# Kernel tuning notes

Hardware: AMD Instinct MI355X
Metric: run time of the kernel (lower is better)

Reference implementation:

```python
import jax, jax.numpy as jnp
import numpy as np

DECAY = 0.99
EPS = 1e-5


def setup_inputs() -> dict:
    key = jax.random.key(0)
    k1, k2 = jax.random.split(key)
    inp = jax.random.normal(k1, (32, 64, 64, 64), dtype=jnp.float32)  # [B,H,W,dim]
    embed = jax.random.normal(k2, (64, 512), dtype=jnp.float32)       # [dim, n_embed]
    cluster_size = jnp.zeros((512,), dtype=jnp.float32)
    embed_avg = embed  # buffer initialized as embed.clone() in torch
    return {"input": inp, "embed": embed, "cluster_size": cluster_size, "embed_avg": embed_avg}


def reference(input, embed, cluster_size, embed_avg):
    dim, n_embed = embed.shape
    flatten = input.reshape(-1, dim)  # [N, dim]

    # pairwise squared distances via ||f||^2 - 2 f.E + ||E||^2 -> [N, n_embed]
    dist = ((flatten ** 2).sum(1, keepdims=True)
            - 2.0 * flatten @ embed
            + (embed ** 2).sum(0, keepdims=True))
    embed_ind_flat = jnp.argmin(dist, axis=1)  # [N] (== argmax of -dist)

    # codebook lookup (F.embedding on embed.T)
    quantize = jnp.take(embed.T, embed_ind_flat, axis=0).reshape(input.shape)

    # EMA stats: one-hot sum and one-hot @ flatten expressed as scatter-adds
    ones = jnp.ones_like(embed_ind_flat, dtype=flatten.dtype)
    embed_onehot_sum = jax.ops.segment_sum(ones, embed_ind_flat, num_segments=n_embed)      # [n_embed]
    embed_sum = jax.ops.segment_sum(flatten, embed_ind_flat, num_segments=n_embed).T       # [dim, n_embed]

    new_cluster_size = cluster_size * DECAY + (1.0 - DECAY) * embed_onehot_sum
    new_embed_avg = embed_avg * DECAY + (1.0 - DECAY) * embed_sum
    n = new_cluster_size.sum()
    cs = (new_cluster_size + EPS) / (n + n_embed * EPS) * n
    new_embed = new_embed_avg / cs[None, :]

    diff = ((jax.lax.stop_gradient(quantize) - input) ** 2).mean()
    quantize_st = input + jax.lax.stop_gradient(quantize - input)  # straight-through
    embed_ind = embed_ind_flat.reshape(input.shape[:-1])

    return (quantize_st, diff, embed_ind, new_cluster_size, new_embed_avg, new_embed)
```

## Files before the change

### kernel.cpp

```cpp
#include <hip/hip_runtime.h>

typedef __attribute__((ext_vector_type(8))) short short8_t;
typedef __attribute__((ext_vector_type(4))) float f32x4;

#define N_ROWS   131072
#define DIM      64
#define NE       512
#define DECAYF   0.99f
#define OMDECAY  0.01f
#define EPSF     1e-5f
#define GAP_THR  0.02f

#define Q_OFF    0
#define DIFF_OFF 8388608
#define IND_OFF  8388609
#define CS_OFF   8519681
#define AVG_OFF  8520193
#define EMB_OFF  8552961

#define WS_ET      0
#define WS_ENORM   32768
#define WS_EN64    33280
#define WS_CSDIV   34304
#define WS_DIFF    34816
#define WS_RCNT    34817
#define WS_IDX     34818
#define WS_RLIST   165890
#define WS_BH      296964
#define WS_BL      313348
#define WS_HIST    329732
#define WS_BINBASE 330244
#define WS_CURSOR  330756
#define WS_SORTED  331268
#define WS_ACCUM   462340

__device__ __forceinline__ ushort f32_to_bf16_rn(float f) {
    unsigned u = __float_as_uint(f);
    unsigned r = (u + 0x7FFFu + ((u >> 16) & 1u)) >> 16;
    return (ushort)r;
}
__device__ __forceinline__ float bf16_to_f32(ushort h) {
    return __uint_as_float(((unsigned)h) << 16);
}

__global__ __launch_bounds__(512) void prep1_kernel(const float* __restrict__ embed,
                                                    float* __restrict__ ws) {
    const int d = blockIdx.x;
    const int c = threadIdx.x;
    float v = embed[d * NE + c];
    ws[WS_ET + c * DIM + d] = v;

    ushort hb = f32_to_bf16_rn(v);
    float  lf = v - bf16_to_f32(hb);
    ushort lb = f32_to_bf16_rn(lf);

    const int T  = c >> 4;
    const int n  = c & 15;
    const int s  = d >> 5;
    const int k8 = (d >> 3) & 3;
    const int jj = d & 7;
    const int l  = k8 * 16 + n;
    const int idx = (T * 2 + s) * 512 + l * 8 + jj;
    ((ushort*)(ws + WS_BH))[idx] = hb;
    ((ushort*)(ws + WS_BL))[idx] = lb;

    if (d == 0 && c == 0) {
        ws[WS_DIFF] = 0.0f;
        ((int*)ws)[WS_RCNT] = 0;
    }
    if (d == 1) ((int*)ws)[WS_HIST + c] = 0;
    ws[WS_ACCUM + blockIdx.x * 512 + threadIdx.x] = 0.0f;
}

__global__ __launch_bounds__(256) void prep2_kernel(float* __restrict__ ws) {
    const int jcode = blockIdx.x * 4 + (threadIdx.x >> 6);
    const int d     = threadIdx.x & 63;
    float v = ws[WS_ET + jcode * DIM + d];
    double sq = (double)v * (double)v;
    #pragma unroll
    for (int off = 32; off > 0; off >>= 1) sq += __shfl_down(sq, off, 64);
    if (d == 0) {
        ws[WS_ENORM + jcode] = (float)sq;
        ((double*)(ws + WS_EN64))[jcode] = sq;
    }
}

__global__ __launch_bounds__(256) void dist_kernel(const float* __restrict__ input,
                                                   float* __restrict__ ws) {
    const int tid  = threadIdx.x;
    const int lane = tid & 63;
    const int wv   = tid >> 6;
    const int r0   = blockIdx.x * 128 + wv * 32;
    const int n15  = lane & 15;
    const int koff = (lane >> 4) * 8;

    short8_t Ahi[2][2], Alo[2][2];
    #pragma unroll
    for (int sub = 0; sub < 2; sub++) {
        const float* rp = input + (size_t)(r0 + sub * 16 + n15) * DIM + koff;
        #pragma unroll
        for (int s = 0; s < 2; s++) {
            float4 x0 = *(const float4*)(rp + s * 32);
            float4 x1 = *(const float4*)(rp + s * 32 + 4);
            float xf[8] = {x0.x, x0.y, x0.z, x0.w, x1.x, x1.y, x1.z, x1.w};
            short8_t h, l;
            #pragma unroll
            for (int e = 0; e < 8; e++) {
                ushort hb = f32_to_bf16_rn(xf[e]);
                float  lf = xf[e] - bf16_to_f32(hb);
                ushort lb = f32_to_bf16_rn(lf);
                h[e] = (short)hb;
                l[e] = (short)lb;
            }
            Ahi[sub][s] = h;
            Alo[sub][s] = l;
        }
    }

    const ushort* bhp = (const ushort*)(ws + WS_BH) + lane * 8;
    const ushort* blp = (const ushort*)(ws + WS_BL) + lane * 8;

    float m1[8], m2[8];
    int   j1[8];
    #pragma unroll
    for (int i = 0; i < 8; i++) { m1[i] = 3.4e38f; m2[i] = 3.4e38f; j1[i] = 0; }

    #pragma unroll 2
    for (int T = 0; T < 32; T++) {
        short8_t Bh0 = *(const short8_t*)(bhp + T * 1024);
        short8_t Bh1 = *(const short8_t*)(bhp + T * 1024 + 512);
        short8_t Bl0 = *(const short8_t*)(blp + T * 1024);
        short8_t Bl1 = *(const short8_t*)(blp + T * 1024 + 512);

        f32x4 aa = {0.f, 0.f, 0.f, 0.f};
        f32x4 ab = {0.f, 0.f, 0.f, 0.f};
        aa = __builtin_amdgcn_mfma_f32_16x16x32_bf16(Ahi[0][0], Bh0, aa, 0, 0, 0);
        ab = __builtin_amdgcn_mfma_f32_16x16x32_bf16(Ahi[1][0], Bh0, ab, 0, 0, 0);
        aa = __builtin_amdgcn_mfma_f32_16x16x32_bf16(Alo[0][0], Bh0, aa, 0, 0, 0);
        ab = __builtin_amdgcn_mfma_f32_16x16x32_bf16(Alo[1][0], Bh0, ab, 0, 0, 0);
        aa = __builtin_amdgcn_mfma_f32_16x16x32_bf16(Ahi[0][0], Bl0, aa, 0, 0, 0);
        ab = __builtin_amdgcn_mfma_f32_16x16x32_bf16(Ahi[1][0], Bl0, ab, 0, 0, 0);
        aa = __builtin_amdgcn_mfma_f32_16x16x32_bf16(Ahi[0][1], Bh1, aa, 0, 0, 0);
        ab = __builtin_amdgcn_mfma_f32_16x16x32_bf16(Ahi[1][1], Bh1, ab, 0, 0, 0);
        aa = __builtin_amdgcn_mfma_f32_16x16x32_bf16(Alo[0][1], Bh1, aa, 0, 0, 0);
        ab = __builtin_amdgcn_mfma_f32_16x16x32_bf16(Alo[1][1], Bh1, ab, 0, 0, 0);
        aa = __builtin_amdgcn_mfma_f32_16x16x32_bf16(Ahi[0][1], Bl1, aa, 0, 0, 0);
        ab = __builtin_amdgcn_mfma_f32_16x16x32_bf16(Ahi[1][1], Bl1, ab, 0, 0, 0);

        const float en = ws[WS_ENORM + T * 16 + n15];
        const int   jc = T * 16 + n15;
        #pragma unroll
        for (int q = 0; q < 4; q++) {
            float da = fmaf(-2.0f, aa[q], en);
            m2[q]    = fminf(m2[q], fmaxf(m1[q], da));
            j1[q]    = (da < m1[q]) ? jc : j1[q];
            m1[q]    = fminf(m1[q], da);
            float db = fmaf(-2.0f, ab[q], en);
            m2[q+4]  = fminf(m2[q+4], fmaxf(m1[q+4], db));
            j1[q+4]  = (db < m1[q+4]) ? jc : j1[q+4];
            m1[q+4]  = fminf(m1[q+4], db);
        }
    }

    #pragma unroll
    for (int off = 1; off < 16; off <<= 1) {
        #pragma unroll
        for (int i = 0; i < 8; i++) {
            float b1 = __shfl_xor(m1[i], off, 64);
            float b2 = __shfl_xor(m2[i], off, 64);
            int   bj = __shfl_xor(j1[i], off, 64);
            float a1 = m1[i];
            float nm2 = fminf(fminf(m2[i], b2), fmaxf(a1, b1));
            bool takeB = (b1 < a1) || (b1 == a1 && bj < j1[i]);
            m1[i] = takeB ? b1 : a1;
            j1[i] = takeB ? bj : j1[i];
            m2[i] = nm2;
        }
    }

    if (n15 == 0) {
        #pragma unroll
        for (int i = 0; i < 8; i++) {
            int sub = i >> 2, q = i & 3;
            int r = r0 + sub * 16 + (lane >> 4) * 4 + q;
            ((int*)ws)[WS_IDX + r] = j1[i];
            if (m2[i] - m1[i] < GAP_THR) {
                int pos = atomicAdd((int*)ws + WS_RCNT, 1);
                ((int*)ws)[WS_RLIST + pos] = r;
            }
        }
    }
}

__global__ __launch_bounds__(256) void refine_kernel(const float* __restrict__ input,
                                                     float* __restrict__ ws) {
    __shared__ float rowf[4][DIM];
    const int cnt  = ((const int*)ws)[WS_RCNT];
    const int lane = threadIdx.x & 63;
    const int wv   = threadIdx.x >> 6;
    const double* en64 = (const double*)(ws + WS_EN64);

    for (int ii = blockIdx.x * 4 + wv; ii < cnt; ii += 2048) {
        const int r = ((const int*)ws)[WS_RLIST + ii];
        rowf[wv][lane] = input[(size_t)r * DIM + lane];
        double bd = 1e300;
        int    bj = 0x7fffffff;
        for (int kk = 0; kk < 8; kk++) {
            int j = kk * 64 + lane;
            const float* ep = ws + WS_ET + j * DIM;
            double s0 = 0.0, s1 = 0.0;
            #pragma unroll 8
            for (int d = 0; d < DIM; d += 2) {
                s0 = fma((double)ep[d],     (double)rowf[wv][d],     s0);
                s1 = fma((double)ep[d + 1], (double)rowf[wv][d + 1], s1);
            }
            double dist = en64[j] - 2.0 * (s0 + s1);
            if (dist < bd || (dist == bd && j < bj)) { bd = dist; bj = j; }
        }
        #pragma unroll
        for (int off = 32; off > 0; off >>= 1) {
            double od = __shfl_down(bd, off, 64);
            int    oj = __shfl_down(bj, off, 64);
            if (od < bd || (od == bd && oj < bj)) { bd = od; bj = oj; }
        }
        if (lane == 0) ((int*)ws)[WS_IDX + r] = bj;
    }
}

__global__ __launch_bounds__(256) void hist_kernel(float* __restrict__ ws) {
    __shared__ int hist[NE];
    const int tid = threadIdx.x;
    for (int e = tid; e < NE; e += 256) hist[e] = 0;
    __syncthreads();

    const int4 j4 = *((const int4*)((const int*)ws + WS_IDX) + blockIdx.x * 256 + tid);
    atomicAdd(&hist[j4.x], 1);
    atomicAdd(&hist[j4.y], 1);
    atomicAdd(&hist[j4.z], 1);
    atomicAdd(&hist[j4.w], 1);
    __syncthreads();

    for (int e = tid; e < NE; e += 256) {
        int h = hist[e];
        if (h) atomicAdd((int*)ws + WS_HIST + e, h);
    }
}

__global__ __launch_bounds__(512) void scanfin_kernel(const float* __restrict__ cluster_size,
                                                      float* __restrict__ ws,
                                                      float* __restrict__ out) {
    __shared__ int wsums[8];
    __shared__ float red[8];
    const int t    = threadIdx.x;
    const int lane = t & 63;
    const int wv   = t >> 6;
    const int v    = ((const int*)ws)[WS_HIST + t];
    const float csnew = fmaf(cluster_size[t], DECAYF, OMDECAY * (float)v);
    out[CS_OFF + t] = csnew;

    int x = v;
    #pragma unroll
    for (int off = 1; off < 64; off <<= 1) {
        int y = __shfl_up(x, off, 64);
        if (lane >= off) x += y;
    }
    if (lane == 63) wsums[wv] = x;

    float s = csnew;
    #pragma unroll
    for (int off = 32; off > 0; off >>= 1) s += __shfl_down(s, off, 64);
    if (lane == 0) red[wv] = s;
    __syncthreads();

    int add = 0;
    for (int w = 0; w < wv; w++) add += wsums[w];
    const int excl = x + add - v;
    ((int*)ws)[WS_BINBASE + t] = excl;
    ((int*)ws)[WS_CURSOR + t]  = excl;

    float n = red[0] + red[1] + red[2] + red[3] + red[4] + red[5] + red[6] + red[7];
    ws[WS_CSDIV + t] = (csnew + EPSF) / (n + (float)NE * EPSF) * n;
}

__global__ __launch_bounds__(256) void place_kernel(float* __restrict__ ws) {
    __shared__ int lhist[NE];
    __shared__ int lbase[NE];
    __shared__ int lcur[NE];
    const int tid  = threadIdx.x;
    const int base = blockIdx.x * 256;

    for (int e = tid; e < NE; e += 256) { lhist[e] = 0; lcur[e] = 0; }
    __syncthreads();

    const int r = base + tid;
    const int j = ((const int*)ws)[WS_IDX + r];
    atomicAdd(&lhist[j], 1);
    __syncthreads();

    for (int e = tid; e < NE; e += 256)
        if (lhist[e]) lbase[e] = atomicAdd((int*)ws + WS_CURSOR + e, lhist[e]);
    __syncthreads();

    const int pos = lbase[j] + atomicAdd(&lcur[j], 1);
    ((int*)ws)[WS_SORTED + pos] = r;
}

__global__ __launch_bounds__(256) void sum_kernel(const float* __restrict__ input,
                                                  float* __restrict__ ws,
                                                  float* __restrict__ out) {
    const int lane = threadIdx.x & 63;
    const int wv   = threadIdx.x >> 6;
    const int i0   = (blockIdx.x * 4 + wv) * 64;

    const int rv = ((const int*)ws)[WS_SORTED + i0 + lane];
    const int jv = ((const int*)ws)[WS_IDX + rv];

    float acc  = 0.0f;
    float dacc = 0.0f;
    int   jcur = __shfl(jv, 0, 64);

    for (int k = 0; k < 64; k += 4) {
        int r0 = __shfl(rv, k,     64);
        int r1 = __shfl(rv, k + 1, 64);
        int r2 = __shfl(rv, k + 2, 64);
        int r3 = __shfl(rv, k + 3, 64);
        float v0 = input[(size_t)r0 * DIM + lane];
        float v1 = input[(size_t)r1 * DIM + lane];
        float v2 = input[(size_t)r2 * DIM + lane];
        float v3 = input[(size_t)r3 * DIM + lane];
        int j0 = __shfl(jv, k,     64);
        int j1 = __shfl(jv, k + 1, 64);
        int j2 = __shfl(jv, k + 2, 64);
        int j3 = __shfl(jv, k + 3, 64);

        float q0 = ws[WS_ET + j0 * DIM + lane];
        float q1 = ws[WS_ET + j1 * DIM + lane];
        float q2 = ws[WS_ET + j2 * DIM + lane];
        float q3 = ws[WS_ET + j3 * DIM + lane];

        out[Q_OFF + (size_t)r0 * DIM + lane] = q0;
        out[Q_OFF + (size_t)r1 * DIM + lane] = q1;
        out[Q_OFF + (size_t)r2 * DIM + lane] = q2;
        out[Q_OFF + (size_t)r3 * DIM + lane] = q3;

        float d0 = q0 - v0, d1 = q1 - v1, d2 = q2 - v2, d3 = q3 - v3;
        dacc = fmaf(d0, d0, fmaf(d1, d1, fmaf(d2, d2, fmaf(d3, d3, dacc))));

        if (lane == 0) {
            out[IND_OFF + r0] = (float)j0;
            out[IND_OFF + r1] = (float)j1;
            out[IND_OFF + r2] = (float)j2;
            out[IND_OFF + r3] = (float)j3;
        }

        if (j0 != jcur) { atomicAdd(&ws[WS_ACCUM + jcur * DIM + lane], acc); acc = 0.0f; jcur = j0; }
        acc += v0;
        if (j1 != jcur) { atomicAdd(&ws[WS_ACCUM + jcur * DIM + lane], acc); acc = 0.0f; jcur = j1; }
        acc += v1;
        if (j2 != jcur) { atomicAdd(&ws[WS_ACCUM + jcur * DIM + lane], acc); acc = 0.0f; jcur = j2; }
        acc += v2;
        if (j3 != jcur) { atomicAdd(&ws[WS_ACCUM + jcur * DIM + lane], acc); acc = 0.0f; jcur = j3; }
        acc += v3;
    }
    atomicAdd(&ws[WS_ACCUM + jcur * DIM + lane], acc);

    #pragma unroll
    for (int off = 1; off < 64; off <<= 1) dacc += __shfl_xor(dacc, off, 64);
    if (lane == 0) atomicAdd(&ws[WS_DIFF], dacc);
}

__global__ __launch_bounds__(512) void emaout_kernel(const float* __restrict__ embed_avg,
                                                     const float* __restrict__ ws,
                                                     float* __restrict__ out) {
    const int e = blockIdx.x * 512 + threadIdx.x;
    const int d = e >> 9;
    const int j = e & (NE - 1);
    float s   = ws[WS_ACCUM + j * DIM + d];
    float avg = fmaf(embed_avg[e], DECAYF, OMDECAY * s);
    out[AVG_OFF + e] = avg;
    out[EMB_OFF + e] = avg / ws[WS_CSDIV + j];
    if (e == 0) out[DIFF_OFF] = ws[WS_DIFF] * (1.0f / 8388608.0f);
}

extern "C" void kernel_launch(void* const* d_in, const int* in_sizes, int n_in,
                              void* d_out, int out_size, void* d_ws, size_t ws_size,
                              hipStream_t stream) {
    const float* input        = (const float*)d_in[0];
    const float* embed        = (const float*)d_in[1];
    const float* cluster_size = (const float*)d_in[2];
    const float* embed_avg    = (const float*)d_in[3];
    float* out = (float*)d_out;
    float* ws  = (float*)d_ws;

    prep1_kernel<<<64, 512, 0, stream>>>(embed, ws);
    prep2_kernel<<<128, 256, 0, stream>>>(ws);
    dist_kernel<<<N_ROWS / 128, 256, 0, stream>>>(input, ws);
    refine_kernel<<<512, 256, 0, stream>>>(input, ws);
    hist_kernel<<<128, 256, 0, stream>>>(ws);
    scanfin_kernel<<<1, 512, 0, stream>>>(cluster_size, ws, out);
    place_kernel<<<512, 256, 0, stream>>>(ws);
    sum_kernel<<<512, 256, 0, stream>>>(input, ws, out);
    emaout_kernel<<<64, 512, 0, stream>>>(embed_avg, ws, out);
}
```

Baseline: 132.7 us.

## Pack codebook index into distance low bits and split sum kernel finer

The distance kernel now packs the 9-bit codebook index into the low mantissa bits of each distance, so tracking the best and second-best entries needs only fminf and fmed3 with no separate index registers or compare-selects. The cross-lane reduction drops the index shuffle and tie-break logic. Because the packing truncates the distances, the near-tie threshold for exact refinement is raised, which sends more rows to the refine kernel. Separately, sum_kernel gives each wave 16 sorted rows instead of 64 and launches four times as many blocks, for more parallelism in the scatter-sum stage.

```diff
diff --git a/kernel.cpp b/kernel.cpp
--- a/kernel.cpp
+++ b/kernel.cpp
@@ -9,7 +9,7 @@
 #define DECAYF   0.99f
 #define OMDECAY  0.01f
 #define EPSF     1e-5f
-#define GAP_THR  0.02f
+#define GAP_THR  0.06f
 
 #define Q_OFF    0
 #define DIFF_OFF 8388608
@@ -121,9 +121,8 @@
     const ushort* blp = (const ushort*)(ws + WS_BL) + lane * 8;
 
     float m1[8], m2[8];
-    int   j1[8];
-    #pragma unroll
-    for (int i = 0; i < 8; i++) { m1[i] = 3.4e38f; m2[i] = 3.4e38f; j1[i] = 0; }
+    #pragma unroll
+    for (int i = 0; i < 8; i++) { m1[i] = 3.4e38f; m2[i] = 3.4e38f; }
 
     #pragma unroll 2
     for (int T = 0; T < 32; T++) {
@@ -147,18 +146,18 @@
         aa = __builtin_amdgcn_mfma_f32_16x16x32_bf16(Ahi[0][1], Bl1, aa, 0, 0, 0);
         ab = __builtin_amdgcn_mfma_f32_16x16x32_bf16(Ahi[1][1], Bl1, ab, 0, 0, 0);
 
-        const float en = ws[WS_ENORM + T * 16 + n15];
-        const int   jc = T * 16 + n15;
+        const float    en = ws[WS_ENORM + T * 16 + n15];
+        const unsigned jc = (unsigned)(T * 16 + n15);
         #pragma unroll
         for (int q = 0; q < 4; q++) {
             float da = fmaf(-2.0f, aa[q], en);
-            m2[q]    = fminf(m2[q], fmaxf(m1[q], da));
-            j1[q]    = (da < m1[q]) ? jc : j1[q];
-            m1[q]    = fminf(m1[q], da);
+            float pa = __uint_as_float((__float_as_uint(da) & 0xFFFFFE00u) | jc);
+            m2[q]   = __builtin_amdgcn_fmed3f(m1[q], m2[q], pa);
+            m1[q]   = fminf(m1[q], pa);
             float db = fmaf(-2.0f, ab[q], en);
-            m2[q+4]  = fminf(m2[q+4], fmaxf(m1[q+4], db));
-            j1[q+4]  = (db < m1[q+4]) ? jc : j1[q+4];
-            m1[q+4]  = fminf(m1[q+4], db);
+            float pb = __uint_as_float((__float_as_uint(db) & 0xFFFFFE00u) | jc);
+            m2[q+4] = __builtin_amdgcn_fmed3f(m1[q+4], m2[q+4], pb);
+            m1[q+4] = fminf(m1[q+4], pb);
         }
     }
 
@@ -166,15 +165,11 @@
     for (int off = 1; off < 16; off <<= 1) {
         #pragma unroll
         for (int i = 0; i < 8; i++) {
-            float b1 = __shfl_xor(m1[i], off, 64);
-            float b2 = __shfl_xor(m2[i], off, 64);
-            int   bj = __shfl_xor(j1[i], off, 64);
-            float a1 = m1[i];
-            float nm2 = fminf(fminf(m2[i], b2), fmaxf(a1, b1));
-            bool takeB = (b1 < a1) || (b1 == a1 && bj < j1[i]);
-            m1[i] = takeB ? b1 : a1;
-            j1[i] = takeB ? bj : j1[i];
-            m2[i] = nm2;
+            float o1 = __shfl_xor(m1[i], off, 64);
+            float o2 = __shfl_xor(m2[i], off, 64);
+            float mx = fmaxf(m1[i], o1);
+            m1[i] = fminf(m1[i], o1);
+            m2[i] = fminf(fminf(m2[i], o2), mx);
         }
     }
 
@@ -183,8 +178,11 @@
         for (int i = 0; i < 8; i++) {
             int sub = i >> 2, q = i & 3;
             int r = r0 + sub * 16 + (lane >> 4) * 4 + q;
-            ((int*)ws)[WS_IDX + r] = j1[i];
-            if (m2[i] - m1[i] < GAP_THR) {
+            const unsigned mb = __float_as_uint(m1[i]);
+            ((int*)ws)[WS_IDX + r] = (int)(mb & 511u);
+            float g1 = __uint_as_float(mb & 0xFFFFFE00u);
+            float g2 = __uint_as_float(__float_as_uint(m2[i]) & 0xFFFFFE00u);
+            if (g2 - g1 < GAP_THR) {
                 int pos = atomicAdd((int*)ws + WS_RCNT, 1);
                 ((int*)ws)[WS_RLIST + pos] = r;
             }
@@ -310,16 +308,17 @@
                                                   float* __restrict__ out) {
     const int lane = threadIdx.x & 63;
     const int wv   = threadIdx.x >> 6;
-    const int i0   = (blockIdx.x * 4 + wv) * 64;
-
-    const int rv = ((const int*)ws)[WS_SORTED + i0 + lane];
+    const int i0   = (blockIdx.x * 4 + wv) * 16;
+
+    const int rv = ((const int*)ws)[WS_SORTED + i0 + (lane & 15)];
     const int jv = ((const int*)ws)[WS_IDX + rv];
 
     float acc  = 0.0f;
     float dacc = 0.0f;
     int   jcur = __shfl(jv, 0, 64);
 
-    for (int k = 0; k < 64; k += 4) {
+    #pragma unroll
+    for (int k = 0; k < 16; k += 4) {
         int r0 = __shfl(rv, k,     64);
         int r1 = __shfl(rv, k + 1, 64);
         int r2 = __shfl(rv, k + 2, 64);
@@ -399,6 +398,6 @@
     hist_kernel<<<128, 256, 0, stream>>>(ws);
     scanfin_kernel<<<1, 512, 0, stream>>>(cluster_size, ws, out);
     place_kernel<<<512, 256, 0, stream>>>(ws);
-    sum_kernel<<<512, 256, 0, stream>>>(input, ws, out);
+    sum_kernel<<<N_ROWS / 64, 256, 0, stream>>>(input, ws, out);
     emaout_kernel<<<64, 512, 0, stream>>>(embed_avg, ws, out);
 }
```

After: 229.0 us. +72.6%, slower.
